# Kernel tuning notes

Measured on AMD Instinct MI355X. Metric: run time of the kernel, lower is better.

## Reference

```python
import jax, jax.numpy as jnp
import numpy as np

N_NODES = 50000
N_EDGES = 400000
NODE_DIM = 128
EDGE_DIM = 64
MSG_DIM = 128
EPS = 1e-5


def _linear_init(key, out_f, in_f):
    kw, kb = jax.random.split(key)
    bound = 1.0 / np.sqrt(in_f)
    W = jax.random.uniform(kw, (out_f, in_f), jnp.float32, -bound, bound)
    b = jax.random.uniform(kb, (out_f,), jnp.float32, -bound, bound)
    return W, b


def setup_inputs() -> dict:
    key = jax.random.key(0)
    ks = jax.random.split(key, 10)
    node_features = jax.random.normal(ks[0], (N_NODES, NODE_DIM), jnp.float32)
    edge_features = jax.random.normal(ks[1], (N_EDGES, EDGE_DIM), jnp.float32)
    edge_indices = jax.random.randint(ks[2], (2, N_EDGES), 0, N_NODES, jnp.int64 if jax.config.jax_enable_x64 else jnp.int32)
    cat_dim = 2 * NODE_DIM + EDGE_DIM  # 320
    Wm1, bm1 = _linear_init(ks[3], MSG_DIM, cat_dim)
    Wm2, bm2 = _linear_init(ks[4], MSG_DIM, MSG_DIM)
    Wm3, bm3 = _linear_init(ks[5], MSG_DIM, MSG_DIM)
    We1, be1 = _linear_init(ks[6], EDGE_DIM, cat_dim)
    We2, be2 = _linear_init(ks[7], EDGE_DIM, EDGE_DIM)
    Wn, bn = _linear_init(ks[8], NODE_DIM, NODE_DIM + MSG_DIM)
    gamma = jnp.ones((NODE_DIM,), jnp.float32)
    beta = jnp.zeros((NODE_DIM,), jnp.float32)
    return {
        'node_features': node_features,
        'edge_features': edge_features,
        'edge_indices': edge_indices,
        'Wm1': Wm1, 'bm1': bm1, 'Wm2': Wm2, 'bm2': bm2, 'Wm3': Wm3, 'bm3': bm3,
        'We1': We1, 'be1': be1, 'We2': We2, 'be2': be2,
        'Wn': Wn, 'bn': bn, 'gamma': gamma, 'beta': beta,
    }


def reference(node_features, edge_features, edge_indices,
              Wm1, bm1, Wm2, bm2, Wm3, bm3,
              We1, be1, We2, be2,
              Wn, bn, gamma, beta):
    src, dst = edge_indices[0], edge_indices[1]
    # [E, 2*node_dim + edge_dim]: gathered endpoints + edge feature
    h = jnp.concatenate([node_features[src], node_features[dst], edge_features], axis=-1)
    # message MLP: Linear-ReLU-Linear-ReLU-Linear
    m = jax.nn.relu(h @ Wm1.T + bm1)
    m = jax.nn.relu(m @ Wm2.T + bm2)
    m = m @ Wm3.T + bm3  # [E, msg_dim]
    # scatter-add messages to destination nodes
    messages = jax.ops.segment_sum(m, dst, num_segments=node_features.shape[0])
    # edge update MLP: Linear-ReLU-Linear
    e = jax.nn.relu(h @ We1.T + be1)
    updated_edges = e @ We2.T + be2
    # node update: Linear-ReLU-LayerNorm
    u = jax.nn.relu(jnp.concatenate([node_features, messages], axis=-1) @ Wn.T + bn)
    mu = jnp.mean(u, axis=-1, keepdims=True)
    var = jnp.mean(jnp.square(u - mu), axis=-1, keepdims=True)
    updated_nodes = (u - mu) * jax.lax.rsqrt(var + EPS) * gamma + beta
    return updated_nodes, updated_edges
```

## Files before the change

### kernel.cpp

```cpp
#include <hip/hip_runtime.h>

#define N_EDGES 400000
#define N_NODES 50000
#define ND 128
#define ED 64
#define MD 128
#define CAT 320
#define ET 64
#define MPITCH 136
#define EPITCH 72
#define H2PITCH 264

typedef unsigned short u16;
typedef __attribute__((ext_vector_type(8))) short bf16x8;
typedef __attribute__((ext_vector_type(4))) float f32x4;

#define WS_WM1 0
#define WS_WM2 40960
#define WS_WM3 57344
#define WS_WE1 73728
#define WS_WE2 94208
#define WS_WN  98304
#define WS_WEND 131072
#define WS_NFB 131072
#define WS_FULL_BYTES (2u * (WS_NFB + N_NODES * ND))

__device__ __forceinline__ u16 f2bf(float f) {
  unsigned int x = __float_as_uint(f);
  unsigned int r = (x + 0x7fffu + ((x >> 16) & 1u)) >> 16;
  return (u16)r;
}
__device__ __forceinline__ bf16x8 ld8f(const float* p) {
  f32x4 a = *(const f32x4*)p;
  f32x4 b = *(const f32x4*)(p + 4);
  bf16x8 r;
  r[0] = (short)f2bf(a[0]); r[1] = (short)f2bf(a[1]);
  r[2] = (short)f2bf(a[2]); r[3] = (short)f2bf(a[3]);
  r[4] = (short)f2bf(b[0]); r[5] = (short)f2bf(b[1]);
  r[6] = (short)f2bf(b[2]); r[7] = (short)f2bf(b[3]);
  return r;
}
template<bool WB>
__device__ __forceinline__ bf16x8 ldw(const void* w, size_t off) {
  if (WB) return *(const bf16x8*)((const u16*)w + off);
  else    return ld8f((const float*)w + off);
}
__device__ __forceinline__ int clampi(int v, int hi) {
  v = v < 0 ? 0 : v;
  return v >= hi ? hi - 1 : v;
}

__global__ __launch_bounds__(256) void prep_weights(
    const float* __restrict__ Wm1, const float* __restrict__ Wm2,
    const float* __restrict__ Wm3, const float* __restrict__ We1,
    const float* __restrict__ We2, const float* __restrict__ Wn,
    u16* __restrict__ ws)
{
  int i = blockIdx.x * 256 + threadIdx.x;
  if (i >= WS_WEND) return;
  const float* s; int off;
  if      (i < WS_WM2) { s = Wm1; off = WS_WM1; }
  else if (i < WS_WM3) { s = Wm2; off = WS_WM2; }
  else if (i < WS_WE1) { s = Wm3; off = WS_WM3; }
  else if (i < WS_WE2) { s = We1; off = WS_WE1; }
  else if (i < WS_WN)  { s = We2; off = WS_WE2; }
  else                 { s = Wn;  off = WS_WN;  }
  ws[i] = f2bf(s[i - off]);
}

__global__ __launch_bounds__(256) void prep_nf(
    const float* __restrict__ nf, u16* __restrict__ nfb)
{
  size_t t = ((size_t)blockIdx.x * 256 + threadIdx.x) * 8;
  if (t >= (size_t)N_NODES * ND) return;
  *(bf16x8*)(nfb + t) = ld8f(nf + t);
}

__device__ __forceinline__ void load_indices(
    int* sIdx, int* sFlag, const void* idxRaw, int eb, int tid)
{
  if (tid < ET) {
    unsigned w = ((const unsigned*)idxRaw)[2u * (unsigned)(eb + tid) + 1u];
    int any32 = __any(w != 0u);
    if (tid == 0) *sFlag = any32;
  }
  __syncthreads();
  const bool is32 = (*sFlag != 0);
  if (tid < ET) {
    int v = is32 ? ((const int*)idxRaw)[eb + tid]
                 : (int)((const long long*)idxRaw)[eb + tid];
    sIdx[tid] = clampi(v, N_NODES);
  } else if (tid < 2 * ET) {
    int t = tid - ET;
    int v = is32 ? ((const int*)idxRaw)[N_EDGES + eb + t]
                 : (int)((const long long*)idxRaw)[(size_t)N_EDGES + eb + t];
    sIdx[tid] = clampi(v, N_NODES);
  }
  __syncthreads();
}

template<bool NB>
__device__ __forceinline__ void gather_h(
    u16* sH, const int* sIdx, const float* __restrict__ nf,
    const u16* __restrict__ nfb, const float* __restrict__ ef,
    int eb, int tid)
{
#pragma unroll
  for (int i = 0; i < 10; ++i) {
    unsigned g = i * 256 + tid;
    unsigned e = g / 40u;
    unsigned c = g - e * 40u;
    bf16x8 v;
    if (c < 32u) {
      int node = sIdx[(c < 16u) ? e : (ET + e)];
      unsigned cc = c & 15u;
      if (NB) v = *(const bf16x8*)(nfb + (size_t)node * ND + cc * 8u);
      else    v = ld8f(nf + (size_t)node * ND + cc * 8u);
    } else {
      v = ld8f(ef + (size_t)(eb + e) * ED + (c - 32u) * 8u);
    }
    unsigned pc = c ^ (e & 7u);
    *(bf16x8*)&sH[e * CAT + pc * 8u] = v;
  }
}

template<bool WB, bool NB>
__global__ __launch_bounds__(256, 3) void edge_fused_kernel(
    const float* __restrict__ nf, const u16* __restrict__ nfb,
    const float* __restrict__ ef, const void* __restrict__ idxRaw,
    const void* __restrict__ wm1, const float* __restrict__ bm1,
    const void* __restrict__ wm2, const float* __restrict__ bm2,
    const void* __restrict__ wm3, const float* __restrict__ bm3,
    const void* __restrict__ we1, const float* __restrict__ be1,
    const void* __restrict__ we2, const float* __restrict__ be2,
    float* __restrict__ msg, float* __restrict__ outE)
{
  __shared__ __align__(16) u16 sH[ET * CAT];
  __shared__ int sIdx[2 * ET];
  __shared__ int sFlag;
  u16* sM = sH;
  u16* sE1 = sH + ET * MPITCH;

  const int tid  = threadIdx.x;
  const int lane = tid & 63;
  const int wave = tid >> 6;
  const int l15  = lane & 15;
  const int quad = lane >> 4;
  const int eb   = blockIdx.x * ET;

  load_indices(sIdx, &sFlag, idxRaw, eb, tid);
  gather_h<NB>(sH, sIdx, nf, nfb, ef, eb, tid);
  __syncthreads();

  f32x4 acc1[3][4] = {};
  for (int kk = 0; kk < 10; ++kk) {
    int ko = kk * 32 + quad * 8;
    unsigned cc = (unsigned)(ko >> 3);
    bf16x8 a[4];
#pragma unroll
    for (int m = 0; m < 4; ++m) {
      unsigned e = (unsigned)(m * 16 + l15);
      a[m] = *(const bf16x8*)&sH[e * CAT + (cc ^ (e & 7u)) * 8u];
    }
#pragma unroll
    for (int i = 0; i < 3; ++i) {
      int nt = 3 * wave + i;
      int f = nt * 16 + l15;
      bf16x8 b = (nt < 8) ? ldw<WB>(wm1, (size_t)f * CAT + ko)
                          : ldw<WB>(we1, (size_t)(f - ND) * CAT + ko);
#pragma unroll
      for (int m = 0; m < 4; ++m)
        acc1[i][m] = __builtin_amdgcn_mfma_f32_16x16x32_bf16(a[m], b, acc1[i][m], 0, 0, 0);
    }
  }
  __syncthreads();

#pragma unroll
  for (int i = 0; i < 3; ++i) {
    int nt = 3 * wave + i;
    int f = nt * 16 + l15;
    float bias = (nt < 8) ? bm1[f] : be1[f - ND];
#pragma unroll
    for (int m = 0; m < 4; ++m)
#pragma unroll
      for (int r = 0; r < 4; ++r) {
        int row = m * 16 + quad * 4 + r;
        float v = acc1[i][m][r] + bias;
        v = v > 0.f ? v : 0.f;
        if (nt < 8) sM[row * MPITCH + f] = f2bf(v);
        else        sE1[row * EPITCH + (f - ND)] = f2bf(v);
      }
  }
  __syncthreads();

  {
    f32x4 acc[4] = {};
    const int f = wave * 16 + l15;
    for (int kk = 0; kk < 2; ++kk) {
      int ko = kk * 32 + quad * 8;
      bf16x8 b = ldw<WB>(we2, (size_t)f * ED + ko);
#pragma unroll
      for (int m = 0; m < 4; ++m) {
        bf16x8 a = *(const bf16x8*)&sE1[(m * 16 + l15) * EPITCH + ko];
        acc[m] = __builtin_amdgcn_mfma_f32_16x16x32_bf16(a, b, acc[m], 0, 0, 0);
      }
    }
    float bias = be2[f];
#pragma unroll
    for (int m = 0; m < 4; ++m)
#pragma unroll
      for (int r = 0; r < 4; ++r) {
        int row = m * 16 + quad * 4 + r;
        outE[(size_t)(eb + row) * ED + f] = acc[m][r] + bias;
      }
  }

  f32x4 acc2[2][4] = {};
  for (int kk = 0; kk < 4; ++kk) {
    int ko = kk * 32 + quad * 8;
    bf16x8 a[4];
#pragma unroll
    for (int m = 0; m < 4; ++m)
      a[m] = *(const bf16x8*)&sM[(m * 16 + l15) * MPITCH + ko];
#pragma unroll
    for (int i = 0; i < 2; ++i) {
      int f = (2 * wave + i) * 16 + l15;
      bf16x8 b = ldw<WB>(wm2, (size_t)f * MD + ko);
#pragma unroll
      for (int m = 0; m < 4; ++m)
        acc2[i][m] = __builtin_amdgcn_mfma_f32_16x16x32_bf16(a[m], b, acc2[i][m], 0, 0, 0);
    }
  }
  __syncthreads();

#pragma unroll
  for (int i = 0; i < 2; ++i) {
    int f = (2 * wave + i) * 16 + l15;
    float bias = bm2[f];
#pragma unroll
    for (int m = 0; m < 4; ++m)
#pragma unroll
      for (int r = 0; r < 4; ++r) {
        int row = m * 16 + quad * 4 + r;
        float v = acc2[i][m][r] + bias;
        sM[row * MPITCH + f] = f2bf(v > 0.f ? v : 0.f);
      }
  }
  __syncthreads();

  f32x4 acc3[2][4] = {};
  for (int kk = 0; kk < 4; ++kk) {
    int ko = kk * 32 + quad * 8;
    bf16x8 a[4];
#pragma unroll
    for (int m = 0; m < 4; ++m)
      a[m] = *(const bf16x8*)&sM[(m * 16 + l15) * MPITCH + ko];
#pragma unroll
    for (int i = 0; i < 2; ++i) {
      int f = (2 * wave + i) * 16 + l15;
      bf16x8 b = ldw<WB>(wm3, (size_t)f * MD + ko);
#pragma unroll
      for (int m = 0; m < 4; ++m)
        acc3[i][m] = __builtin_amdgcn_mfma_f32_16x16x32_bf16(a[m], b, acc3[i][m], 0, 0, 0);
    }
  }
#pragma unroll
  for (int i = 0; i < 2; ++i) {
    int f = (2 * wave + i) * 16 + l15;
    float bias = bm3[f];
#pragma unroll
    for (int m = 0; m < 4; ++m)
#pragma unroll
      for (int r = 0; r < 4; ++r) {
        int row = m * 16 + quad * 4 + r;
        int d = sIdx[ET + row];
        atomicAdd(&msg[(size_t)d * MD + f], acc3[i][m][r] + bias);
      }
  }
}

template<bool WB, bool NB>
__global__ __launch_bounds__(256, 4) void node_kernel(
    const float* __restrict__ nf, const u16* __restrict__ nfb,
    const float* __restrict__ msg,
    const void* __restrict__ wn, const float* __restrict__ bn,
    const float* __restrict__ gamma, const float* __restrict__ beta,
    float* __restrict__ outN)
{
  __shared__ __align__(16) u16 sH[ET * H2PITCH];
  __shared__ float sPart[4][ET][2];

  const int tid  = threadIdx.x;
  const int lane = tid & 63;
  const int wave = tid >> 6;
  const int l15  = lane & 15;
  const int quad = lane >> 4;
  const int nb   = blockIdx.x * ET;

#pragma unroll
  for (int i = 0; i < 8; ++i) {
    int g = i * 256 + tid;
    int r = g >> 5;
    int c = g & 31;
    int node = nb + r;
    bool valid = node < N_NODES;
    bf16x8 v = {};
    if (c < 16) {
      if (valid) {
        if (NB) v = *(const bf16x8*)(nfb + (size_t)node * ND + c * 8);
        else    v = ld8f(nf + (size_t)node * ND + c * 8);
      }
      *(bf16x8*)&sH[r * H2PITCH + c * 8] = v;
    } else {
      int co = (c - 16) * 8;
      if (valid) v = ld8f(msg + (size_t)node * MD + co);
      *(bf16x8*)&sH[r * H2PITCH + ND + co] = v;
    }
  }
  __syncthreads();

  f32x4 acc[2][4] = {};
  for (int kk = 0; kk < 8; ++kk) {
    int ko = kk * 32 + quad * 8;
    bf16x8 a[4];
#pragma unroll
    for (int m = 0; m < 4; ++m)
      a[m] = *(const bf16x8*)&sH[(m * 16 + l15) * H2PITCH + ko];
#pragma unroll
    for (int i = 0; i < 2; ++i) {
      int f = (2 * wave + i) * 16 + l15;
      bf16x8 b = ldw<WB>(wn, (size_t)f * 256 + ko);
#pragma unroll
      for (int m = 0; m < 4; ++m)
        acc[i][m] = __builtin_amdgcn_mfma_f32_16x16x32_bf16(a[m], b, acc[i][m], 0, 0, 0);
    }
  }

#pragma unroll
  for (int i = 0; i < 2; ++i) {
    int f = (2 * wave + i) * 16 + l15;
    float bias = bn[f];
#pragma unroll
    for (int m = 0; m < 4; ++m)
#pragma unroll
      for (int r = 0; r < 4; ++r) {
        float v = acc[i][m][r] + bias;
        acc[i][m][r] = v > 0.f ? v : 0.f;
      }
  }

#pragma unroll
  for (int m = 0; m < 4; ++m)
#pragma unroll
    for (int r = 0; r < 4; ++r) {
      float p = acc[0][m][r] + acc[1][m][r];
      float q = acc[0][m][r] * acc[0][m][r] + acc[1][m][r] * acc[1][m][r];
#pragma unroll
      for (int mk = 1; mk < 16; mk <<= 1) {
        p += __shfl_xor(p, mk);
        q += __shfl_xor(q, mk);
      }
      if (l15 == 0) {
        int row = m * 16 + quad * 4 + r;
        sPart[wave][row][0] = p;
        sPart[wave][row][1] = q;
      }
    }
  __syncthreads();

#pragma unroll
  for (int m = 0; m < 4; ++m)
#pragma unroll
    for (int r = 0; r < 4; ++r) {
      int row = m * 16 + quad * 4 + r;
      float ts  = sPart[0][row][0] + sPart[1][row][0] + sPart[2][row][0] + sPart[3][row][0];
      float tss = sPart[0][row][1] + sPart[1][row][1] + sPart[2][row][1] + sPart[3][row][1];
      float mu  = ts * 0.0078125f;
      float var = tss * 0.0078125f - mu * mu;
      var = var > 0.f ? var : 0.f;
      float rstd = rsqrtf(var + 1e-5f);
      int node = nb + row;
      if (node < N_NODES) {
#pragma unroll
        for (int i = 0; i < 2; ++i) {
          int f = (2 * wave + i) * 16 + l15;
          float o = (acc[i][m][r] - mu) * rstd * gamma[f] + beta[f];
          outN[(size_t)node * ND + f] = o;
        }
      }
    }
}

extern "C" void kernel_launch(void* const* d_in, const int* in_sizes, int n_in,
                              void* d_out, int out_size, void* d_ws, size_t ws_size,
                              hipStream_t stream)
{
  const float* nf  = (const float*)d_in[0];
  const float* ef  = (const float*)d_in[1];
  const void*  ei  = d_in[2];
  const float* Wm1 = (const float*)d_in[3];
  const float* bm1 = (const float*)d_in[4];
  const float* Wm2 = (const float*)d_in[5];
  const float* bm2 = (const float*)d_in[6];
  const float* Wm3 = (const float*)d_in[7];
  const float* bm3 = (const float*)d_in[8];
  const float* We1 = (const float*)d_in[9];
  const float* be1 = (const float*)d_in[10];
  const float* We2 = (const float*)d_in[11];
  const float* be2 = (const float*)d_in[12];
  const float* Wn  = (const float*)d_in[13];
  const float* bn  = (const float*)d_in[14];
  const float* gamma = (const float*)d_in[15];
  const float* beta  = (const float*)d_in[16];

  float* outN = (float*)d_out;
  float* outE = outN + (size_t)N_NODES * ND;
  float* msg  = outN;

  const bool haveW  = ws_size >= (size_t)(2u * WS_WEND);
  const bool haveNF = ws_size >= (size_t)WS_FULL_BYTES;
  u16* ws = (u16*)d_ws;
  const u16* nfb = ws + WS_NFB;

  hipMemsetAsync(msg, 0, (size_t)N_NODES * MD * sizeof(float), stream);

  if (haveW) {
    prep_weights<<<(WS_WEND + 255) / 256, 256, 0, stream>>>(
        Wm1, Wm2, Wm3, We1, We2, Wn, ws);
    if (haveNF)
      prep_nf<<<(N_NODES * ND / 8 + 255) / 256, 256, 0, stream>>>(nf, ws + WS_NFB);
  }

  const int egrid = N_EDGES / ET;
  const int ngrid = (N_NODES + ET - 1) / ET;

  if (haveW && haveNF) {
    edge_fused_kernel<true, true><<<egrid, 256, 0, stream>>>(
        nf, nfb, ef, ei,
        ws + WS_WM1, bm1, ws + WS_WM2, bm2, ws + WS_WM3, bm3,
        ws + WS_WE1, be1, ws + WS_WE2, be2, msg, outE);
    node_kernel<true, true><<<ngrid, 256, 0, stream>>>(
        nf, nfb, msg, ws + WS_WN, bn, gamma, beta, outN);
  } else if (haveW) {
    edge_fused_kernel<true, false><<<egrid, 256, 0, stream>>>(
        nf, nullptr, ef, ei,
        ws + WS_WM1, bm1, ws + WS_WM2, bm2, ws + WS_WM3, bm3,
        ws + WS_WE1, be1, ws + WS_WE2, be2, msg, outE);
    node_kernel<true, false><<<ngrid, 256, 0, stream>>>(
        nf, nullptr, msg, ws + WS_WN, bn, gamma, beta, outN);
  } else {
    edge_fused_kernel<false, false><<<egrid, 256, 0, stream>>>(
        nf, nullptr, ef, ei,
        Wm1, bm1, Wm2, bm2, Wm3, bm3, We1, be1, We2, be2, msg, outE);
    node_kernel<false, false><<<ngrid, 256, 0, stream>>>(
        nf, nullptr, msg, Wn, bn, gamma, beta, outN);
  }
}
```

Before: 620.7 us.

## Bucket edges by destination block and fuse edge MLP with node update

Adds a counting sort of edges into 782 buckets of 64 destination nodes (count, scan, fill kernels). A single bucket kernel then runs the edge MLPs for each bucket's edges in chunks of 16, accumulates messages in shared memory with LDS atomics, and applies the node linear layer and LayerNorm in the same block. This removes the global message memset, the global atomic scatter and the separate node kernel. The cost is three extra small launches, load imbalance from uneven bucket sizes, and 16-edge MFMA tiles that make poorer use of the matrix units than the old 64-edge tiles.

```diff
diff --git a/kernel.cpp b/kernel.cpp
--- a/kernel.cpp
+++ b/kernel.cpp
@@ -10,6 +10,8 @@
 #define MPITCH 136
 #define EPITCH 72
 #define H2PITCH 264
+#define CE 16
+#define NBKT 782
 
 typedef unsigned short u16;
 typedef __attribute__((ext_vector_type(8))) short bf16x8;
@@ -23,7 +25,10 @@
 #define WS_WN  98304
 #define WS_WEND 131072
 #define WS_NFB 131072
-#define WS_FULL_BYTES (2u * (WS_NFB + N_NODES * ND))
+#define WS_CSR (WS_NFB + N_NODES * ND)
+#define WS_FULL_BYTES (2u * (unsigned)WS_CSR)
+#define CSR_INTS (NBKT + (NBKT + 1) + NBKT + N_EDGES)
+#define WS_BKT_BYTES (2u * (unsigned)WS_CSR + 4u * (unsigned)CSR_INTS)
 
 __device__ __forceinline__ u16 f2bf(float f) {
   unsigned int x = __float_as_uint(f);
@@ -74,6 +79,353 @@
   size_t t = ((size_t)blockIdx.x * 256 + threadIdx.x) * 8;
   if (t >= (size_t)N_NODES * ND) return;
   *(bf16x8*)(nfb + t) = ld8f(nf + t);
+}
+
+__device__ __forceinline__ bool detect32(const void* idxRaw, int lane) {
+  unsigned w = ((const unsigned*)idxRaw)[2 * lane + 1];
+  return __any(w != 0u) != 0;
+}
+
+__global__ __launch_bounds__(256) void count_kernel(
+    const void* __restrict__ idxRaw, int* __restrict__ cnt)
+{
+  const bool is32 = detect32(idxRaw, threadIdx.x & 63);
+  int e = blockIdx.x * 256 + threadIdx.x;
+  if (e < N_EDGES) {
+    int d = is32 ? ((const int*)idxRaw)[N_EDGES + e]
+                 : (int)((const long long*)idxRaw)[(size_t)N_EDGES + e];
+    d = clampi(d, N_NODES);
+    atomicAdd(&cnt[d >> 6], 1);
+  }
+}
+
+__global__ __launch_bounds__(64) void scan_kernel(
+    const int* __restrict__ cnt, int* __restrict__ boff, int* __restrict__ cur)
+{
+  int lane = threadIdx.x;
+  int loc[13]; int s = 0;
+#pragma unroll
+  for (int i = 0; i < 13; ++i) {
+    int b = lane * 13 + i;
+    loc[i] = s;
+    s += (b < NBKT) ? cnt[b] : 0;
+  }
+  int inc = s;
+  for (int d = 1; d < 64; d <<= 1) {
+    int v = __shfl_up(inc, d);
+    if (lane >= d) inc += v;
+  }
+  int excl = inc - s;
+#pragma unroll
+  for (int i = 0; i < 13; ++i) {
+    int b = lane * 13 + i;
+    if (b < NBKT) { int o = excl + loc[i]; boff[b] = o; cur[b] = o; }
+  }
+  if (lane == 63) boff[NBKT] = inc;
+}
+
+__global__ __launch_bounds__(256) void fill_kernel(
+    const void* __restrict__ idxRaw, int* __restrict__ cur,
+    int* __restrict__ permArr)
+{
+  const bool is32 = detect32(idxRaw, threadIdx.x & 63);
+  int e = blockIdx.x * 256 + threadIdx.x;
+  if (e < N_EDGES) {
+    int d = is32 ? ((const int*)idxRaw)[N_EDGES + e]
+                 : (int)((const long long*)idxRaw)[(size_t)N_EDGES + e];
+    d = clampi(d, N_NODES);
+    int p = atomicAdd(&cur[d >> 6], 1);
+    permArr[p] = e;
+  }
+}
+
+__global__ __launch_bounds__(256, 3) void bucket_kernel(
+    const u16* __restrict__ nfb, const float* __restrict__ ef,
+    const void* __restrict__ idxRaw,
+    const u16* __restrict__ wm1, const float* __restrict__ bm1,
+    const u16* __restrict__ wm2, const float* __restrict__ bm2,
+    const u16* __restrict__ wm3, const float* __restrict__ bm3,
+    const u16* __restrict__ we1, const float* __restrict__ be1,
+    const u16* __restrict__ we2, const float* __restrict__ be2,
+    const u16* __restrict__ wn,  const float* __restrict__ bn,
+    const float* __restrict__ gamma, const float* __restrict__ beta,
+    const int* __restrict__ boff, const int* __restrict__ perm,
+    float* __restrict__ outN, float* __restrict__ outE)
+{
+  __shared__ __align__(16) u16 sH[CE * 256];
+  __shared__ __align__(16) float sMsg[ET][MD];
+  __shared__ int sEid[2][CE];
+  __shared__ int sSrc[2][CE];
+  __shared__ int sDst[2][CE];
+  __shared__ float sPart[4][ET][2];
+
+  const int tid  = threadIdx.x;
+  const int lane = tid & 63;
+  const int wave = tid >> 6;
+  const int l15  = lane & 15;
+  const int quad = lane >> 4;
+  const int b    = blockIdx.x;
+  const int nb   = b * ET;
+
+  for (int i = tid; i < ET * MD; i += 256) ((float*)sMsg)[i] = 0.f;
+
+  const bool is32 = detect32(idxRaw, lane);
+  const int e0 = boff[b];
+  int nE = boff[b + 1] - e0;
+  nE = nE < 0 ? 0 : (nE > N_EDGES ? N_EDGES : nE);
+  const int nCh = (nE + CE - 1) / CE;
+
+  u16* sM  = sH;
+  u16* sE1 = sH + CE * MPITCH;
+
+  if (tid < CE && nCh > 0) {
+    int q = tid;
+    int p = e0 + (q < nE ? q : 0);
+    int eId = perm[p];
+    int s, d;
+    if (is32) {
+      s = ((const int*)idxRaw)[eId];
+      d = ((const int*)idxRaw)[N_EDGES + eId];
+    } else {
+      s = (int)((const long long*)idxRaw)[eId];
+      d = (int)((const long long*)idxRaw)[(size_t)N_EDGES + eId];
+    }
+    sEid[0][tid] = eId;
+    sSrc[0][tid] = clampi(s, N_NODES);
+    sDst[0][tid] = clampi(d, N_NODES) & (ET - 1);
+  }
+  __syncthreads();
+
+  for (int ch = 0; ch < nCh; ++ch) {
+    const int cb = ch & 1;
+    int n = nE - ch * CE; n = n > CE ? CE : n;
+
+    if (tid < CE && ch + 1 < nCh) {
+      int q = (ch + 1) * CE + tid;
+      int p = e0 + (q < nE ? q : 0);
+      int eId = perm[p];
+      int s, d;
+      if (is32) {
+        s = ((const int*)idxRaw)[eId];
+        d = ((const int*)idxRaw)[N_EDGES + eId];
+      } else {
+        s = (int)((const long long*)idxRaw)[eId];
+        d = (int)((const long long*)idxRaw)[(size_t)N_EDGES + eId];
+      }
+      sEid[cb ^ 1][tid] = eId;
+      sSrc[cb ^ 1][tid] = clampi(s, N_NODES);
+      sDst[cb ^ 1][tid] = clampi(d, N_NODES) & (ET - 1);
+    }
+
+#pragma unroll
+    for (int i = 0; i < 2; ++i) {
+      int g = i * 256 + tid;
+      int e = g >> 5, c = g & 31;
+      int node = (c < 16) ? sSrc[cb][e] : (nb + sDst[cb][e]);
+      int cc = c & 15;
+      bf16x8 v = *(const bf16x8*)(nfb + (size_t)node * ND + cc * 8);
+      int pc = c ^ (e & 7);
+      *(bf16x8*)&sH[e * 256 + pc * 8] = v;
+    }
+    __syncthreads();
+
+    const int myEid = sEid[cb][l15];
+
+    f32x4 acc1[3] = {};
+    for (int kk = 0; kk < 10; ++kk) {
+      int ko = kk * 32 + quad * 8;
+      bf16x8 a;
+      if (kk < 8) {
+        int cc = ko >> 3;
+        a = *(const bf16x8*)&sH[l15 * 256 + ((cc ^ (l15 & 7)) * 8)];
+      } else {
+        a = ld8f(ef + (size_t)myEid * ED + (ko - 256));
+      }
+#pragma unroll
+      for (int i = 0; i < 3; ++i) {
+        int nt = 3 * wave + i;
+        int f = nt * 16 + l15;
+        bf16x8 bb = (nt < 8)
+          ? *(const bf16x8*)(wm1 + (size_t)f * CAT + ko)
+          : *(const bf16x8*)(we1 + (size_t)(f - ND) * CAT + ko);
+        acc1[i] = __builtin_amdgcn_mfma_f32_16x16x32_bf16(a, bb, acc1[i], 0, 0, 0);
+      }
+    }
+    __syncthreads();
+
+#pragma unroll
+    for (int i = 0; i < 3; ++i) {
+      int nt = 3 * wave + i;
+      int f = nt * 16 + l15;
+      float bias = (nt < 8) ? bm1[f] : be1[f - ND];
+#pragma unroll
+      for (int r = 0; r < 4; ++r) {
+        int row = quad * 4 + r;
+        float v = acc1[i][r] + bias;
+        v = v > 0.f ? v : 0.f;
+        if (nt < 8) sM[row * MPITCH + f] = f2bf(v);
+        else        sE1[row * EPITCH + (f - ND)] = f2bf(v);
+      }
+    }
+    __syncthreads();
+
+    {
+      f32x4 acc = {};
+      int f = wave * 16 + l15;
+#pragma unroll
+      for (int kk = 0; kk < 2; ++kk) {
+        int ko = kk * 32 + quad * 8;
+        bf16x8 bb = *(const bf16x8*)(we2 + (size_t)f * ED + ko);
+        bf16x8 a = *(const bf16x8*)&sE1[l15 * EPITCH + ko];
+        acc = __builtin_amdgcn_mfma_f32_16x16x32_bf16(a, bb, acc, 0, 0, 0);
+      }
+      float bias = be2[f];
+#pragma unroll
+      for (int r = 0; r < 4; ++r) {
+        int row = quad * 4 + r;
+        if (row < n) {
+          int eId = sEid[cb][row];
+          outE[(size_t)eId * ED + f] = acc[r] + bias;
+        }
+      }
+    }
+
+    f32x4 acc2[2] = {};
+    for (int kk = 0; kk < 4; ++kk) {
+      int ko = kk * 32 + quad * 8;
+      bf16x8 a = *(const bf16x8*)&sM[l15 * MPITCH + ko];
+#pragma unroll
+      for (int i = 0; i < 2; ++i) {
+        int f = (2 * wave + i) * 16 + l15;
+        bf16x8 bb = *(const bf16x8*)(wm2 + (size_t)f * MD + ko);
+        acc2[i] = __builtin_amdgcn_mfma_f32_16x16x32_bf16(a, bb, acc2[i], 0, 0, 0);
+      }
+    }
+    __syncthreads();
+#pragma unroll
+    for (int i = 0; i < 2; ++i) {
+      int f = (2 * wave + i) * 16 + l15;
+      float bias = bm2[f];
+#pragma unroll
+      for (int r = 0; r < 4; ++r) {
+        int row = quad * 4 + r;
+        float v = acc2[i][r] + bias;
+        sM[row * MPITCH + f] = f2bf(v > 0.f ? v : 0.f);
+      }
+    }
+    __syncthreads();
+
+    f32x4 acc3[2] = {};
+    for (int kk = 0; kk < 4; ++kk) {
+      int ko = kk * 32 + quad * 8;
+      bf16x8 a = *(const bf16x8*)&sM[l15 * MPITCH + ko];
+#pragma unroll
+      for (int i = 0; i < 2; ++i) {
+        int f = (2 * wave + i) * 16 + l15;
+        bf16x8 bb = *(const bf16x8*)(wm3 + (size_t)f * MD + ko);
+        acc3[i] = __builtin_amdgcn_mfma_f32_16x16x32_bf16(a, bb, acc3[i], 0, 0, 0);
+      }
+    }
+#pragma unroll
+    for (int r = 0; r < 4; ++r) {
+      int row = quad * 4 + r;
+      if (row < n) {
+        int dloc = sDst[cb][row];
+#pragma unroll
+        for (int i = 0; i < 2; ++i) {
+          int f = (2 * wave + i) * 16 + l15;
+          atomicAdd(&sMsg[dloc][f], acc3[i][r] + bm3[f]);
+        }
+      }
+    }
+    __syncthreads();
+  }
+
+  f32x4 acc[2][4] = {};
+  for (int kk = 0; kk < 8; ++kk) {
+    int ko = kk * 32 + quad * 8;
+    bf16x8 a[4];
+#pragma unroll
+    for (int m = 0; m < 4; ++m) {
+      int e = m * 16 + l15;
+      if (kk < 4) {
+        int node = nb + e; node = node < N_NODES ? node : N_NODES - 1;
+        a[m] = *(const bf16x8*)(nfb + (size_t)node * ND + ko);
+      } else {
+        const float* p = &sMsg[e][ko - 128];
+        f32x4 x = *(const f32x4*)p;
+        f32x4 y = *(const f32x4*)(p + 4);
+        bf16x8 t;
+        t[0] = (short)f2bf(x[0]); t[1] = (short)f2bf(x[1]);
+        t[2] = (short)f2bf(x[2]); t[3] = (short)f2bf(x[3]);
+        t[4] = (short)f2bf(y[0]); t[5] = (short)f2bf(y[1]);
+        t[6] = (short)f2bf(y[2]); t[7] = (short)f2bf(y[3]);
+        a[m] = t;
+      }
+    }
+#pragma unroll
+    for (int i = 0; i < 2; ++i) {
+      int f = (2 * wave + i) * 16 + l15;
+      bf16x8 bb = *(const bf16x8*)(wn + (size_t)f * 256 + ko);
+#pragma unroll
+      for (int m = 0; m < 4; ++m)
+        acc[i][m] = __builtin_amdgcn_mfma_f32_16x16x32_bf16(a[m], bb, acc[i][m], 0, 0, 0);
+    }
+  }
+
+#pragma unroll
+  for (int i = 0; i < 2; ++i) {
+    int f = (2 * wave + i) * 16 + l15;
+    float bias = bn[f];
+#pragma unroll
+    for (int m = 0; m < 4; ++m)
+#pragma unroll
+      for (int r = 0; r < 4; ++r) {
+        float v = acc[i][m][r] + bias;
+        acc[i][m][r] = v > 0.f ? v : 0.f;
+      }
+  }
+
+#pragma unroll
+  for (int m = 0; m < 4; ++m)
+#pragma unroll
+    for (int r = 0; r < 4; ++r) {
+      float p = acc[0][m][r] + acc[1][m][r];
+      float q = acc[0][m][r] * acc[0][m][r] + acc[1][m][r] * acc[1][m][r];
+#pragma unroll
+      for (int mk = 1; mk < 16; mk <<= 1) {
+        p += __shfl_xor(p, mk);
+        q += __shfl_xor(q, mk);
+      }
+      if (l15 == 0) {
+        int row = m * 16 + quad * 4 + r;
+        sPart[wave][row][0] = p;
+        sPart[wave][row][1] = q;
+      }
+    }
+  __syncthreads();
+
+#pragma unroll
+  for (int m = 0; m < 4; ++m)
+#pragma unroll
+    for (int r = 0; r < 4; ++r) {
+      int row = m * 16 + quad * 4 + r;
+      float ts  = sPart[0][row][0] + sPart[1][row][0] + sPart[2][row][0] + sPart[3][row][0];
+      float tss = sPart[0][row][1] + sPart[1][row][1] + sPart[2][row][1] + sPart[3][row][1];
+      float mu  = ts * 0.0078125f;
+      float var = tss * 0.0078125f - mu * mu;
+      var = var > 0.f ? var : 0.f;
+      float rstd = rsqrtf(var + 1e-5f);
+      int node = nb + row;
+      if (node < N_NODES) {
+#pragma unroll
+        for (int i = 0; i < 2; ++i) {
+          int f = (2 * wave + i) * 16 + l15;
+          float o = (acc[i][m][r] - mu) * rstd * gamma[f] + beta[f];
+          outN[(size_t)node * ND + f] = o;
+        }
+      }
+    }
 }
 
 __device__ __forceinline__ void load_indices(
@@ -415,14 +767,12 @@
 
   float* outN = (float*)d_out;
   float* outE = outN + (size_t)N_NODES * ND;
-  float* msg  = outN;
-
-  const bool haveW  = ws_size >= (size_t)(2u * WS_WEND);
-  const bool haveNF = ws_size >= (size_t)WS_FULL_BYTES;
+
+  const bool haveW   = ws_size >= (size_t)(2u * WS_WEND);
+  const bool haveNF  = ws_size >= (size_t)WS_FULL_BYTES;
+  const bool haveBkt = ws_size >= (size_t)WS_BKT_BYTES;
   u16* ws = (u16*)d_ws;
   const u16* nfb = ws + WS_NFB;
-
-  hipMemsetAsync(msg, 0, (size_t)N_NODES * MD * sizeof(float), stream);
 
   if (haveW) {
     prep_weights<<<(WS_WEND + 255) / 256, 256, 0, stream>>>(
@@ -430,6 +780,28 @@
     if (haveNF)
       prep_nf<<<(N_NODES * ND / 8 + 255) / 256, 256, 0, stream>>>(nf, ws + WS_NFB);
   }
+
+  if (haveBkt) {
+    int* csr     = (int*)(ws + WS_CSR);
+    int* cnt     = csr;
+    int* boff    = csr + NBKT;
+    int* cur     = boff + NBKT + 1;
+    int* permArr = cur + NBKT;
+
+    hipMemsetAsync(cnt, 0, NBKT * sizeof(int), stream);
+    count_kernel<<<(N_EDGES + 255) / 256, 256, 0, stream>>>(ei, cnt);
+    scan_kernel<<<1, 64, 0, stream>>>(cnt, boff, cur);
+    fill_kernel<<<(N_EDGES + 255) / 256, 256, 0, stream>>>(ei, cur, permArr);
+    bucket_kernel<<<NBKT, 256, 0, stream>>>(
+        nfb, ef, ei,
+        ws + WS_WM1, bm1, ws + WS_WM2, bm2, ws + WS_WM3, bm3,
+        ws + WS_WE1, be1, ws + WS_WE2, be2, ws + WS_WN, bn,
+        gamma, beta, boff, permArr, outN, outE);
+    return;
+  }
+
+  float* msg = outN;
+  hipMemsetAsync(msg, 0, (size_t)N_NODES * MD * sizeof(float), stream);
 
   const int egrid = N_EDGES / ET;
   const int ngrid = (N_NODES + ET - 1) / ET;
```

Measured after the change: 1.424 ms. 2.29x slower.
